# Optimization experiments

Hardware: AMD Instinct MI355X
Metric: run time of the kernel (lower is better)

Reference implementation:

```python
import jax, jax.numpy as jnp
import numpy as np

E = 64      # hidden_dim
FF = 128    # ff_dim
H = 4       # nhead
D = E // H  # head_dim = 16
STEPS = 16  # recursion_steps
IN = 200    # input_dim
B = 131072  # batch


def _ln(h, g, b):
    m = h.mean(-1, keepdims=True)
    v = ((h - m) ** 2).mean(-1, keepdims=True)
    return (h - m) * jax.lax.rsqrt(v + 1e-5) * g + b


def _ffn(h, w1, b1, w2, b2):
    return jax.nn.gelu(h @ w1.T + b1, approximate=False) @ w2.T + b2


def _forward(x, W_in, b_in, g_in, be_in,
             z_in_w, z_in_b, z_out_w, z_out_b,
             z_ffn_w1, z_ffn_b1, z_ffn_w2, z_ffn_b2,
             zn1_g, zn1_b, zn2_g, zn2_b,
             y_in_w, y_in_b, y_out_w, y_out_b,
             y_ffn_w1, y_ffn_b1, y_ffn_w2, y_ffn_b2,
             yn1_g, yn1_b, yn2_g, yn2_b,
             W_out, b_out):
    Bn = x.shape[0]
    x_proj = jax.nn.gelu(_ln(x @ W_in.T + b_in, g_in, be_in), approximate=False)  # [B,E]
    y0 = jnp.zeros((Bn, E), dtype=x.dtype)
    z0 = jnp.zeros((Bn, E), dtype=x.dtype)
    scale = 1.0 / np.sqrt(D).astype(np.float32)
    Wv_y = y_in_w[2 * E:]   # cross-attn over a single kv token: softmax weight == 1,
    bv_y = y_in_b[2 * E:]   # so output = out_proj(v_proj(z)) exactly (no approximation)

    def step(carry, _):
        y, z = carry
        seq = jnp.stack([x_proj, y, z], axis=1)            # [B,3,E]
        qkv = seq @ z_in_w.T + z_in_b                      # [B,3,3E]
        q, k, v = jnp.split(qkv, 3, axis=-1)
        rh = lambda t: t.reshape(Bn, 3, H, D).transpose(0, 2, 1, 3)  # [B,H,3,D]
        q, k, v = rh(q), rh(k), rh(v)
        att = jax.nn.softmax(jnp.einsum('bhsd,bhtd->bhst', q, k) * scale, axis=-1)
        o = jnp.einsum('bhst,bhtd->bhsd', att, v).transpose(0, 2, 1, 3).reshape(Bn, 3, E)
        o = o @ z_out_w.T + z_out_b
        z_res = _ln(z + o[:, 2, :], zn1_g, zn1_b)
        z2 = _ln(z_res + _ffn(z_res, z_ffn_w1, z_ffn_b1, z_ffn_w2, z_ffn_b2), zn2_g, zn2_b)
        ca = (z2 @ Wv_y.T + bv_y) @ y_out_w.T + y_out_b    # 1-token cross-attention
        y_res = _ln(y + ca, yn1_g, yn1_b)
        y2 = _ln(y_res + _ffn(y_res, y_ffn_w1, y_ffn_b1, y_ffn_w2, y_ffn_b2), yn2_g, yn2_b)
        return (y2, z2), None

    (y, z), _ = jax.lax.scan(step, (y0, z0), None, length=STEPS)
    return (y @ W_out.T + b_out)[:, 0]                     # [B]


def setup_inputs() -> dict:
    key = jax.random.key(0)
    ks = jax.random.split(key, 12)
    f = lambda k, s: jax.random.normal(k, s, dtype=jnp.float32) * 0.05
    zeros = lambda s: jnp.zeros(s, dtype=jnp.float32)
    ones = lambda s: jnp.ones(s, dtype=jnp.float32)
    return {
        'x': jax.random.normal(ks[0], (B, IN), dtype=jnp.float32),
        'W_in': f(ks[1], (E, IN)), 'b_in': zeros((E,)),
        'g_in': ones((E,)), 'be_in': zeros((E,)),
        'z_in_w': f(ks[2], (3 * E, E)), 'z_in_b': zeros((3 * E,)),
        'z_out_w': f(ks[3], (E, E)), 'z_out_b': zeros((E,)),
        'z_ffn_w1': f(ks[4], (FF, E)), 'z_ffn_b1': zeros((FF,)),
        'z_ffn_w2': f(ks[5], (E, FF)), 'z_ffn_b2': zeros((E,)),
        'zn1_g': ones((E,)), 'zn1_b': zeros((E,)),
        'zn2_g': ones((E,)), 'zn2_b': zeros((E,)),
        'y_in_w': f(ks[6], (3 * E, E)), 'y_in_b': zeros((3 * E,)),
        'y_out_w': f(ks[7], (E, E)), 'y_out_b': zeros((E,)),
        'y_ffn_w1': f(ks[8], (FF, E)), 'y_ffn_b1': zeros((FF,)),
        'y_ffn_w2': f(ks[9], (E, FF)), 'y_ffn_b2': zeros((E,)),
        'yn1_g': ones((E,)), 'yn1_b': zeros((E,)),
        'yn2_g': ones((E,)), 'yn2_b': zeros((E,)),
        'W_out': f(ks[10], (1, E)), 'b_out': zeros((1,)),
    }


def reference(x, W_in, b_in, g_in, be_in,
              z_in_w, z_in_b, z_out_w, z_out_b,
              z_ffn_w1, z_ffn_b1, z_ffn_w2, z_ffn_b2,
              zn1_g, zn1_b, zn2_g, zn2_b,
              y_in_w, y_in_b, y_out_w, y_out_b,
              y_ffn_w1, y_ffn_b1, y_ffn_w2, y_ffn_b2,
              yn1_g, yn1_b, yn2_g, yn2_b,
              W_out, b_out):
    return _forward(x, W_in, b_in, g_in, be_in,
                    z_in_w, z_in_b, z_out_w, z_out_b,
                    z_ffn_w1, z_ffn_b1, z_ffn_w2, z_ffn_b2,
                    zn1_g, zn1_b, zn2_g, zn2_b,
                    y_in_w, y_in_b, y_out_w, y_out_b,
                    y_ffn_w1, y_ffn_b1, y_ffn_w2, y_ffn_b2,
                    yn1_g, yn1_b, yn2_g, yn2_b,
                    W_out, b_out)
```

## Files before the change

### kernel.cpp

```cpp
#include <hip/hip_runtime.h>
#include <math.h>


constexpr int STEPS = 16;
constexpr int INDIM = 200;

typedef __attribute__((ext_vector_type(8))) short bfrag8;
typedef __attribute__((ext_vector_type(4))) float f32x4;
typedef __attribute__((ext_vector_type(4))) short s16x4;

constexpr int FB_WIN  = 0;
constexpr int NFRAG   = 140;
constexpr int NPARAM  = 1544;

constexpr int LB_ZQ   = 0;
constexpr int LB_ZK   = 8;
constexpr int LB_ZV   = 16;
constexpr int LB_ZOUT = 24;
constexpr int LB_ZF1  = 32;
constexpr int LB_ZF2  = 48;
constexpr int LB_YV   = 64;
constexpr int LB_YOUT = 72;
constexpr int LB_YF1  = 80;
constexpr int LB_YF2  = 96;
constexpr int NSTEADY = 112;

constexpr int PB_BIN   = 0;
constexpr int PB_GIN   = 64;
constexpr int PB_BEIN  = 128;
constexpr int PB_ZINB  = 192;
constexpr int PB_ZOUTB = 384;
constexpr int PB_ZF1B  = 448;
constexpr int PB_ZF2B  = 576;
constexpr int PB_ZN1G  = 640;
constexpr int PB_ZN1B  = 704;
constexpr int PB_ZN2G  = 768;
constexpr int PB_ZN2B  = 832;
constexpr int PB_YVB   = 896;
constexpr int PB_YOUTB = 960;
constexpr int PB_YF1B  = 1024;
constexpr int PB_YF2B  = 1152;
constexpr int PB_YN1G  = 1216;
constexpr int PB_YN1B  = 1280;
constexpr int PB_YN2G  = 1344;
constexpr int PB_YN2B  = 1408;
constexpr int PB_WOUT  = 1472;
constexpr int PB_BOUT  = 1536;

constexpr int S64      = 72;
constexpr int L_W      = 0;
constexpr int L_P      = 57344;
constexpr int L_ACT    = 60432;
constexpr int WAVE_SH  = 1152;
constexpr int NWAVE    = 16;
constexpr int ARENA_SH = L_ACT + NWAVE * WAVE_SH;

struct Params {
  const float *x, *W_in, *b_in, *g_in, *be_in;
  const float *z_in_w, *z_in_b, *z_out_w, *z_out_b;
  const float *z_ffn_w1, *z_ffn_b1, *z_ffn_w2, *z_ffn_b2;
  const float *zn1_g, *zn1_b, *zn2_g, *zn2_b;
  const float *y_in_w, *y_in_b, *y_out_w, *y_out_b;
  const float *y_ffn_w1, *y_ffn_b1, *y_ffn_w2, *y_ffn_b2;
  const float *yn1_g, *yn1_b, *yn2_g, *yn2_b;
  const float *W_out, *b_out;
  float *out;
  int nrows;
};

__device__ __forceinline__ ushort f2bf_rne(float f) {
  uint u = __float_as_uint(f);
  u += 0x7FFFu + ((u >> 16) & 1u);
  return (ushort)(u >> 16);
}

__device__ __forceinline__ ushort f2bf(float f) {
  return (ushort)((__float_as_uint(f) + 0x8000u) >> 16);
}
__device__ __forceinline__ uint pk2(float a, float b) {
  uint ua = __float_as_uint(a) + 0x8000u;
  uint ub = __float_as_uint(b) + 0x8000u;
  return (ua >> 16) | (ub & 0xFFFF0000u);
}
__device__ __forceinline__ float upk_lo(uint u) {
  return __uint_as_float(u << 16);
}
__device__ __forceinline__ float upk_hi(uint u) {
  return __uint_as_float(u & 0xFFFF0000u);
}
__device__ __forceinline__ f32x4 upk4(const uint* p) {
  f32x4 r;
  r.x = upk_lo(p[0]); r.y = upk_hi(p[0]);
  r.z = upk_lo(p[1]); r.w = upk_hi(p[1]);
  return r;
}
__device__ __forceinline__ float dot4(f32x4 a, f32x4 b) {
  return a.x * b.x + a.y * b.y + a.z * b.z + a.w * b.w;
}
__device__ __forceinline__ void stc(short* buf, int stride, int mt, int q,
                                    int s, f32x4 c) {
  s16x4 v;
  v.x = (short)f2bf(c.x); v.y = (short)f2bf(c.y);
  v.z = (short)f2bf(c.z); v.w = (short)f2bf(c.w);
  *(s16x4*)(buf + s * stride + mt * 16 + q * 4) = v;
}

__device__ __forceinline__ void c2b_p(const uint p[8], bfrag8& b0, bfrag8& b1,
                                      int lane) {
  const int srcA = (lane & 15) | ((lane & 16) << 1);
  const int srcB = srcA + 16;
  const bool odd = (lane & 32) != 0;
  uint ev0 = p[0], ev1 = p[1], ev2 = p[4], ev3 = p[5];
  uint od0 = p[2], od1 = p[3], od2 = p[6], od3 = p[7];
  uint rA0, rA1, rA2, rA3, rB0, rB1, rB2, rB3;
  {
    uint e, o;
    e = (uint)__shfl((int)ev0, srcA); o = (uint)__shfl((int)od0, srcA); rA0 = odd ? o : e;
    e = (uint)__shfl((int)ev1, srcA); o = (uint)__shfl((int)od1, srcA); rA1 = odd ? o : e;
    e = (uint)__shfl((int)ev2, srcA); o = (uint)__shfl((int)od2, srcA); rA2 = odd ? o : e;
    e = (uint)__shfl((int)ev3, srcA); o = (uint)__shfl((int)od3, srcA); rA3 = odd ? o : e;
    e = (uint)__shfl((int)ev0, srcB); o = (uint)__shfl((int)od0, srcB); rB0 = odd ? o : e;
    e = (uint)__shfl((int)ev1, srcB); o = (uint)__shfl((int)od1, srcB); rB1 = odd ? o : e;
    e = (uint)__shfl((int)ev2, srcB); o = (uint)__shfl((int)od2, srcB); rB2 = odd ? o : e;
    e = (uint)__shfl((int)ev3, srcB); o = (uint)__shfl((int)od3, srcB); rB3 = odd ? o : e;
  }
  union U { uint u[4]; bfrag8 b; };
  U u0, u1;
  u0.u[0] = rA0; u0.u[1] = rA1; u0.u[2] = rB0; u0.u[3] = rB1;
  u1.u[0] = rA2; u1.u[1] = rA3; u1.u[2] = rB2; u1.u[3] = rB3;
  b0 = u0.b; b1 = u1.b;
}
__device__ __forceinline__ void c2b(const f32x4 c[4], bfrag8& b0, bfrag8& b1,
                                    int lane) {
  uint p[8];
#pragma unroll
  for (int mt = 0; mt < 4; ++mt) {
    p[2 * mt]     = pk2(c[mt].x, c[mt].y);
    p[2 * mt + 1] = pk2(c[mt].z, c[mt].w);
  }
  c2b_p(p, b0, b1, lane);
}

template <int MT>
__device__ __forceinline__ void layerN2(const short* in0, const short* in1,
                                        const short* lw, int fbase,
                                        const float* bias, f32x4* c0, f32x4* c1,
                                        int lane, int q, int s) {
  bfrag8 b0[2], b1[2];
#pragma unroll
  for (int kt = 0; kt < 2; ++kt) {
    b0[kt] = *(const bfrag8*)(in0 + s * S64 + kt * 32 + q * 8);
    b1[kt] = *(const bfrag8*)(in1 + s * S64 + kt * 32 + q * 8);
  }
#pragma unroll
  for (int mt = 0; mt < MT; ++mt) {
    f32x4 b4 = *(const f32x4*)(bias + mt * 16 + q * 4);
    c0[mt] = b4; c1[mt] = b4;
  }
#pragma unroll
  for (int mt = 0; mt < MT; ++mt) {
#pragma unroll
    for (int kt = 0; kt < 2; ++kt) {
      bfrag8 af = *(const bfrag8*)(lw + (fbase + mt * 2 + kt) * 512 + lane * 8);
      c0[mt] = __builtin_amdgcn_mfma_f32_16x16x32_bf16(af, b0[kt], c0[mt], 0, 0, 0);
      c1[mt] = __builtin_amdgcn_mfma_f32_16x16x32_bf16(af, b1[kt], c1[mt], 0, 0, 0);
    }
  }
}

template <int MT>
__device__ __forceinline__ void layerB2(const bfrag8* bfA, const bfrag8* bfB,
                                        const short* lw, int fbase,
                                        const float* bias, f32x4* cA, f32x4* cB,
                                        int lane, int q) {
#pragma unroll
  for (int mt = 0; mt < MT; ++mt) {
    f32x4 b4 = *(const f32x4*)(bias + mt * 16 + q * 4);
    cA[mt] = b4; cB[mt] = b4;
  }
#pragma unroll
  for (int mt = 0; mt < MT; ++mt) {
#pragma unroll
    for (int kt = 0; kt < 2; ++kt) {
      bfrag8 af = *(const bfrag8*)(lw + (fbase + mt * 2 + kt) * 512 + lane * 8);
      cA[mt] = __builtin_amdgcn_mfma_f32_16x16x32_bf16(af, bfA[kt], cA[mt], 0, 0, 0);
      cB[mt] = __builtin_amdgcn_mfma_f32_16x16x32_bf16(af, bfB[kt], cB[mt], 0, 0, 0);
    }
  }
}

template <int MT>
__device__ __forceinline__ void layerB4(const bfrag8* bf0, const bfrag8* bf1,
                                        const bfrag8* bf2, const bfrag8* bf3,
                                        const short* lw, int fbase,
                                        const float* bias, f32x4* c0, f32x4* c1,
                                        f32x4* c2, f32x4* c3, int lane, int q) {
#pragma unroll
  for (int mt = 0; mt < MT; ++mt) {
    f32x4 b4 = *(const f32x4*)(bias + mt * 16 + q * 4);
    c0[mt] = b4; c1[mt] = b4; c2[mt] = b4; c3[mt] = b4;
  }
#pragma unroll
  for (int mt = 0; mt < MT; ++mt) {
#pragma unroll
    for (int kt = 0; kt < 2; ++kt) {
      bfrag8 af = *(const bfrag8*)(lw + (fbase + mt * 2 + kt) * 512 + lane * 8);
      c0[mt] = __builtin_amdgcn_mfma_f32_16x16x32_bf16(af, bf0[kt], c0[mt], 0, 0, 0);
      c1[mt] = __builtin_amdgcn_mfma_f32_16x16x32_bf16(af, bf1[kt], c1[mt], 0, 0, 0);
      c2[mt] = __builtin_amdgcn_mfma_f32_16x16x32_bf16(af, bf2[kt], c2[mt], 0, 0, 0);
      c3[mt] = __builtin_amdgcn_mfma_f32_16x16x32_bf16(af, bf3[kt], c3[mt], 0, 0, 0);
    }
  }
}

__device__ __forceinline__ void lnorm_c(f32x4 c[4], const float* g,
                                        const float* b, int q) {
  f32x4 s4 = (c[0] + c[1]) + (c[2] + c[3]);
  float sm = (s4.x + s4.y) + (s4.z + s4.w);
  sm += __shfl_xor(sm, 16); sm += __shfl_xor(sm, 32);
  float mean = sm * (1.f / 64.f);
  f32x4 vs4 = {0.f, 0.f, 0.f, 0.f};
#pragma unroll
  for (int mt = 0; mt < 4; ++mt) {
    f32x4 d = c[mt] - mean;
    c[mt] = d;
    vs4 = vs4 + d * d;
  }
  float vs = (vs4.x + vs4.y) + (vs4.z + vs4.w);
  vs += __shfl_xor(vs, 16); vs += __shfl_xor(vs, 32);
  float rs = rsqrtf(vs * (1.f / 64.f) + 1e-5f);
#pragma unroll
  for (int mt = 0; mt < 4; ++mt) {
    f32x4 g4 = *(const f32x4*)(g + mt * 16 + q * 4);
    f32x4 b4 = *(const f32x4*)(b + mt * 16 + q * 4);
    c[mt] = (c[mt] * rs) * g4 + b4;
  }
}

__device__ __forceinline__ f32x4 gelu4(f32x4 x) {
  const float K = 0.70710678118654752f;
  f32x4 ax;
  ax.x = fabsf(x.x) * K; ax.y = fabsf(x.y) * K;
  ax.z = fabsf(x.z) * K; ax.w = fabsf(x.w) * K;
  f32x4 u = ax * 0.47047f + 1.0f;
  f32x4 t;
  t.x = __builtin_amdgcn_rcpf(u.x); t.y = __builtin_amdgcn_rcpf(u.y);
  t.z = __builtin_amdgcn_rcpf(u.z); t.w = __builtin_amdgcn_rcpf(u.w);
  f32x4 poly = ((t * 0.7478556f + (-0.0958798f)) * t + 0.3480242f) * t;
  f32x4 gq = ax * ax;
  f32x4 e;
  e.x = __expf(-gq.x); e.y = __expf(-gq.y);
  e.z = __expf(-gq.z); e.w = __expf(-gq.w);
  f32x4 r = poly * e;
  f32x4 er;
  er.x = copysignf(1.0f - r.x, x.x); er.y = copysignf(1.0f - r.y, x.y);
  er.z = copysignf(1.0f - r.z, x.z); er.w = copysignf(1.0f - r.w, x.w);
  f32x4 h = x * 0.5f;
  return h + h * er;
}

__device__ __forceinline__ void ffn2_via_th2(const f32x4 h0[8], const f32x4 h1[8],
                                             short* TH0, short* TH1,
                                             const short* lw, int f2base,
                                             const float* b2, f32x4 c0[4],
                                             f32x4 c1[4], int lane, int q, int s) {
#pragma unroll
  for (int mt = 0; mt < 4; ++mt) {
    f32x4 b4 = *(const f32x4*)(b2 + mt * 16 + q * 4);
    c0[mt] = b4; c1[mt] = b4;
  }
#pragma unroll
  for (int g = 0; g < 2; ++g) {
#pragma unroll
    for (int mt = 0; mt < 4; ++mt) {
      stc(TH0, S64, mt, q, s, gelu4(h0[4 * g + mt]));
      stc(TH1, S64, mt, q, s, gelu4(h1[4 * g + mt]));
    }
    bfrag8 bf0[2], bf1[2];
#pragma unroll
    for (int kt = 0; kt < 2; ++kt) {
      bf0[kt] = *(const bfrag8*)(TH0 + s * S64 + kt * 32 + q * 8);
      bf1[kt] = *(const bfrag8*)(TH1 + s * S64 + kt * 32 + q * 8);
    }
#pragma unroll
    for (int mt = 0; mt < 4; ++mt) {
#pragma unroll
      for (int kt = 0; kt < 2; ++kt) {
        bfrag8 af =
            *(const bfrag8*)(lw + (f2base + mt * 4 + 2 * g + kt) * 512 + lane * 8);
        c0[mt] = __builtin_amdgcn_mfma_f32_16x16x32_bf16(af, bf0[kt], c0[mt], 0, 0, 0);
        c1[mt] = __builtin_amdgcn_mfma_f32_16x16x32_bf16(af, bf1[kt], c1[mt], 0, 0, 0);
      }
    }
  }
}

__global__ void prepack_kernel(Params p, ushort* wf) {
  int f = blockIdx.x;
  int lane = threadIdx.x;

  if (f == NFRAG) {
    float* pw = (float*)(wf + (size_t)NFRAG * 512);
    for (int t = lane; t < NPARAM; t += 64) {
      float v = 0.f;
      if      (t < 64)   v = p.b_in[t];
      else if (t < 128)  v = p.g_in[t - 64];
      else if (t < 192)  v = p.be_in[t - 128];
      else if (t < 384)  v = p.z_in_b[t - 192];
      else if (t < 448)  v = p.z_out_b[t - 384];
      else if (t < 576)  v = p.z_ffn_b1[t - 448];
      else if (t < 640)  v = p.z_ffn_b2[t - 576];
      else if (t < 704)  v = p.zn1_g[t - 640];
      else if (t < 768)  v = p.zn1_b[t - 704];
      else if (t < 832)  v = p.zn2_g[t - 768];
      else if (t < 896)  v = p.zn2_b[t - 832];
      else if (t < 960)  v = p.y_in_b[128 + t - 896];
      else if (t < 1024) v = p.y_out_b[t - 960];
      else if (t < 1152) v = p.y_ffn_b1[t - 1024];
      else if (t < 1216) v = p.y_ffn_b2[t - 1152];
      else if (t < 1280) v = p.yn1_g[t - 1216];
      else if (t < 1344) v = p.yn1_b[t - 1280];
      else if (t < 1408) v = p.yn2_g[t - 1344];
      else if (t < 1472) v = p.yn2_b[t - 1408];
      else if (t < 1536) v = p.W_out[t - 1472];
      else if (t == 1536) v = p.b_out[0];
      pw[t] = v;
    }
    return;
  }

  int q = lane >> 4, r = lane & 15;
  const float* src; int K, mt, kt, l;
  if (f < 28)        { src = p.W_in;                K = 200; mt = f / 7;  kt = f % 7; }
  else if (f < 36)   { l = f - 28;  src = p.z_in_w;            K = 64;  mt = l / 2; kt = l % 2; }
  else if (f < 44)   { l = f - 36;  src = p.z_in_w + 64 * 64;  K = 64;  mt = l / 2; kt = l % 2; }
  else if (f < 52)   { l = f - 44;  src = p.z_in_w + 128 * 64; K = 64;  mt = l / 2; kt = l % 2; }
  else if (f < 60)   { l = f - 52;  src = p.z_out_w;           K = 64;  mt = l / 2; kt = l % 2; }
  else if (f < 76)   { l = f - 60;  src = p.z_ffn_w1;          K = 64;  mt = l / 2; kt = l % 2; }
  else if (f < 92)   { l = f - 76;  src = p.z_ffn_w2;          K = 128; mt = l / 4; kt = l % 4; }
  else if (f < 100)  { l = f - 92;  src = p.y_in_w + 128 * 64; K = 64;  mt = l / 2; kt = l % 2; }
  else if (f < 108)  { l = f - 100; src = p.y_out_w;           K = 64;  mt = l / 2; kt = l % 2; }
  else if (f < 124)  { l = f - 108; src = p.y_ffn_w1;          K = 64;  mt = l / 2; kt = l % 2; }
  else               { l = f - 124; src = p.y_ffn_w2;          K = 128; mt = l / 4; kt = l % 4; }

  int row = mt * 16 + r;
  int col = kt * 32 + q * 8;
  bfrag8 o;
#pragma unroll
  for (int j = 0; j < 8; ++j) {
    int cc = col + j;
    float v = (cc < K) ? src[(size_t)row * K + cc] : 0.0f;
    o[j] = (short)f2bf_rne(v);
  }
  *(bfrag8*)(wf + (size_t)f * 512 + lane * 8) = o;
}

__global__ __launch_bounds__(512, 1)
void trm_mfma_kernel(Params p, const ushort* wf) {
  __shared__ __align__(16) short arena[ARENA_SH];
  const int tid = threadIdx.x;
  const int wave = tid >> 6, lane = tid & 63;
  const int q = lane >> 4, s = lane & 15;

  {
    const uint4* srcw = (const uint4*)(wf + (size_t)28 * 512);
    uint4* dstw = (uint4*)(arena + L_W);
    for (int i = tid; i < NSTEADY * 64; i += 512) dstw[i] = srcw[i];
    const uint4* srcp = (const uint4*)(wf + (size_t)NFRAG * 512);
    uint4* dstp = (uint4*)(arena + L_P);
    for (int i = tid; i < NPARAM / 4; i += 512) dstp[i] = srcp[i];
  }
  __syncthreads();

  const short* LW = arena + L_W;
  const float* P  = (const float*)(arena + L_P);
  short* TH0 = arena + L_ACT + (2 * wave) * WAVE_SH;
  short* TH1 = TH0 + WAVE_SH;

  const int chunks = (p.nrows + 255) / 256;
  for (int ic = blockIdx.x; ic < chunks; ic += gridDim.x) {
    int rw[2];
#pragma unroll
    for (int t = 0; t < 2; ++t) {
      int r = ic * 256 + wave * 16 + t * 128 + s;
      rw[t] = (r < p.nrows) ? r : (p.nrows - 1);
    }

    bfrag8 xpB[2][2];
    {
      bfrag8 xb[2][7];
#pragma unroll
      for (int t = 0; t < 2; ++t) {
        const float* xr = p.x + (size_t)rw[t] * INDIM;
#pragma unroll
        for (int kt = 0; kt < 7; ++kt) {
          int k0i = kt * 32 + q * 8;
          bfrag8 v;
          if (kt < 6 || q == 0) {
            f32x4 lo = *(const f32x4*)(xr + k0i);
            f32x4 hi = *(const f32x4*)(xr + k0i + 4);
            v[0] = (short)f2bf(lo.x); v[1] = (short)f2bf(lo.y);
            v[2] = (short)f2bf(lo.z); v[3] = (short)f2bf(lo.w);
            v[4] = (short)f2bf(hi.x); v[5] = (short)f2bf(hi.y);
            v[6] = (short)f2bf(hi.z); v[7] = (short)f2bf(hi.w);
          } else {
#pragma unroll
            for (int j = 0; j < 8; ++j) v[j] = 0;
          }
          xb[t][kt] = v;
        }
      }
      f32x4 c[2][4];
#pragma unroll
      for (int mt = 0; mt < 4; ++mt) {
        f32x4 b4 = *(const f32x4*)(P + PB_BIN + mt * 16 + q * 4);
        c[0][mt] = b4; c[1][mt] = b4;
      }
#pragma unroll
      for (int mt = 0; mt < 4; ++mt)
#pragma unroll
        for (int kt = 0; kt < 7; ++kt) {
          bfrag8 af =
              *(const bfrag8*)(wf + (size_t)(FB_WIN + mt * 7 + kt) * 512 + lane * 8);
          c[0][mt] = __builtin_amdgcn_mfma_f32_16x16x32_bf16(af, xb[0][kt], c[0][mt], 0, 0, 0);
          c[1][mt] = __builtin_amdgcn_mfma_f32_16x16x32_bf16(af, xb[1][kt], c[1][mt], 0, 0, 0);
        }
#pragma unroll
      for (int t = 0; t < 2; ++t) {
        lnorm_c(c[t], P + PB_GIN, P + PB_BEIN, q);
#pragma unroll
        for (int mt = 0; mt < 4; ++mt) c[t][mt] = gelu4(c[t][mt]);
        c2b(c[t], xpB[t][0], xpB[t][1], lane);
      }
    }

    uint k0p[2][8], v0p[2][8], zCp[2][8], yCp[2][8];
    bfrag8 zB[2][2], yB[2][2];
    {
      f32x4 ck[2][4], cv[2][4];
      layerB2<4>(xpB[0], xpB[1], LW, LB_ZK, P + PB_ZINB + 64, ck[0], ck[1], lane, q);
      layerB2<4>(xpB[0], xpB[1], LW, LB_ZV, P + PB_ZINB + 128, cv[0], cv[1], lane, q);
#pragma unroll
      for (int t = 0; t < 2; ++t) {
#pragma unroll
        for (int mt = 0; mt < 4; ++mt) {
          k0p[t][2 * mt]     = pk2(ck[t][mt].x, ck[t][mt].y);
          k0p[t][2 * mt + 1] = pk2(ck[t][mt].z, ck[t][mt].w);
          v0p[t][2 * mt]     = pk2(cv[t][mt].x, cv[t][mt].y);
          v0p[t][2 * mt + 1] = pk2(cv[t][mt].z, cv[t][mt].w);
          zCp[t][2 * mt] = 0u; zCp[t][2 * mt + 1] = 0u;
          yCp[t][2 * mt] = 0u; yCp[t][2 * mt + 1] = 0u;
        }
#pragma unroll
        for (int kt = 0; kt < 2; ++kt) {
          bfrag8 zr0;
#pragma unroll
          for (int j = 0; j < 8; ++j) zr0[j] = 0;
          zB[t][kt] = zr0; yB[t][kt] = zr0;
        }
      }
    }

    for (int st = 0; st < STEPS; ++st) {
      float w0[2][4], w1[2][4], w2[2][4], wi[2][4];
      {
        f32x4 q2[2][4], kz[2][4], ky[2][4];
        layerB2<4>(zB[0], zB[1], LW, LB_ZQ, P + PB_ZINB, q2[0], q2[1], lane, q);
        layerB4<4>(zB[0], yB[0], zB[1], yB[1], LW, LB_ZK, P + PB_ZINB + 64,
                   kz[0], ky[0], kz[1], ky[1], lane, q);
#pragma unroll
        for (int t = 0; t < 2; ++t) {
#pragma unroll
          for (int mt = 0; mt < 4; ++mt) {
            float a0 = dot4(q2[t][mt], upk4(k0p[t] + 2 * mt));
            float a1 = dot4(q2[t][mt], ky[t][mt]);
            float a2 = dot4(q2[t][mt], kz[t][mt]);
            a0 += __shfl_xor(a0, 16); a0 += __shfl_xor(a0, 32);
            a1 += __shfl_xor(a1, 16); a1 += __shfl_xor(a1, 32);
            a2 += __shfl_xor(a2, 16); a2 += __shfl_xor(a2, 32);
            a0 *= 0.25f; a1 *= 0.25f; a2 *= 0.25f;
            float mx = fmaxf(a0, fmaxf(a1, a2));
            float e0 = __expf(a0 - mx), e1 = __expf(a1 - mx), e2 = __expf(a2 - mx);
            w0[t][mt] = e0; w1[t][mt] = e1; w2[t][mt] = e2;
            wi[t][mt] = __builtin_amdgcn_rcpf(e0 + e1 + e2);
          }
        }
      }
      {
        f32x4 vz[2][4], vy[2][4];
        layerB4<4>(zB[0], yB[0], zB[1], yB[1], LW, LB_ZV, P + PB_ZINB + 128,
                   vz[0], vy[0], vz[1], vy[1], lane, q);
#pragma unroll
        for (int mt = 0; mt < 4; ++mt) {
          f32x4 o0 = (upk4(v0p[0] + 2 * mt) * w0[0][mt] + vy[0][mt] * w1[0][mt] +
                      vz[0][mt] * w2[0][mt]) * wi[0][mt];
          stc(TH0, S64, mt, q, s, o0);
          f32x4 o1 = (upk4(v0p[1] + 2 * mt) * w0[1][mt] + vy[1][mt] * w1[1][mt] +
                      vz[1][mt] * w2[1][mt]) * wi[1][mt];
          stc(TH1, S64, mt, q, s, o1);
        }
      }

      uint zrp[2][8];
      {
        f32x4 zr[2][4];
        layerN2<4>(TH0, TH1, LW, LB_ZOUT, P + PB_ZOUTB, zr[0], zr[1], lane, q, s);
#pragma unroll
        for (int t = 0; t < 2; ++t) {
#pragma unroll
          for (int mt = 0; mt < 4; ++mt) zr[t][mt] = zr[t][mt] + upk4(zCp[t] + 2 * mt);
          lnorm_c(zr[t], P + PB_ZN1G, P + PB_ZN1B, q);
        }
#pragma unroll
        for (int mt = 0; mt < 4; ++mt) {
          stc(TH0, S64, mt, q, s, zr[0][mt]);
          stc(TH1, S64, mt, q, s, zr[1][mt]);
        }
#pragma unroll
        for (int t = 0; t < 2; ++t)
#pragma unroll
          for (int mt = 0; mt < 4; ++mt) {
            zrp[t][2 * mt]     = pk2(zr[t][mt].x, zr[t][mt].y);
            zrp[t][2 * mt + 1] = pk2(zr[t][mt].z, zr[t][mt].w);
          }
      }

      f32x4 z2[2][4];
      {
        f32x4 h8[2][8];
        layerN2<8>(TH0, TH1, LW, LB_ZF1, P + PB_ZF1B, h8[0], h8[1], lane, q, s);
        ffn2_via_th2(h8[0], h8[1], TH0, TH1, LW, LB_ZF2, P + PB_ZF2B,
                     z2[0], z2[1], lane, q, s);
      }
#pragma unroll
      for (int t = 0; t < 2; ++t) {
#pragma unroll
        for (int mt = 0; mt < 4; ++mt) z2[t][mt] = z2[t][mt] + upk4(zrp[t] + 2 * mt);
        lnorm_c(z2[t], P + PB_ZN2G, P + PB_ZN2B, q);
        uint zp[8];
#pragma unroll
        for (int mt = 0; mt < 4; ++mt) {
          zp[2 * mt]     = pk2(z2[t][mt].x, z2[t][mt].y);
          zp[2 * mt + 1] = pk2(z2[t][mt].z, z2[t][mt].w);
          zCp[t][2 * mt] = zp[2 * mt]; zCp[t][2 * mt + 1] = zp[2 * mt + 1];
        }
        c2b_p(zp, zB[t][0], zB[t][1], lane);
      }

      {
        f32x4 t4[2][4];
        layerB2<4>(zB[0], zB[1], LW, LB_YV, P + PB_YVB, t4[0], t4[1], lane, q);
#pragma unroll
        for (int mt = 0; mt < 4; ++mt) {
          stc(TH0, S64, mt, q, s, t4[0][mt]);
          stc(TH1, S64, mt, q, s, t4[1][mt]);
        }
      }

      uint yrp[2][8];
      {
        f32x4 yr[2][4];
        layerN2<4>(TH0, TH1, LW, LB_YOUT, P + PB_YOUTB, yr[0], yr[1], lane, q, s);
#pragma unroll
        for (int t = 0; t < 2; ++t) {
#pragma unroll
          for (int mt = 0; mt < 4; ++mt) yr[t][mt] = yr[t][mt] + upk4(yCp[t] + 2 * mt);
          lnorm_c(yr[t], P + PB_YN1G, P + PB_YN1B, q);
        }
#pragma unroll
        for (int mt = 0; mt < 4; ++mt) {
          stc(TH0, S64, mt, q, s, yr[0][mt]);
          stc(TH1, S64, mt, q, s, yr[1][mt]);
        }
#pragma unroll
        for (int t = 0; t < 2; ++t)
#pragma unroll
          for (int mt = 0; mt < 4; ++mt) {
            yrp[t][2 * mt]     = pk2(yr[t][mt].x, yr[t][mt].y);
            yrp[t][2 * mt + 1] = pk2(yr[t][mt].z, yr[t][mt].w);
          }
      }

      f32x4 y2[2][4];
      {
        f32x4 h8[2][8];
        layerN2<8>(TH0, TH1, LW, LB_YF1, P + PB_YF1B, h8[0], h8[1], lane, q, s);
        ffn2_via_th2(h8[0], h8[1], TH0, TH1, LW, LB_YF2, P + PB_YF2B,
                     y2[0], y2[1], lane, q, s);
      }
#pragma unroll
      for (int t = 0; t < 2; ++t) {
#pragma unroll
        for (int mt = 0; mt < 4; ++mt) y2[t][mt] = y2[t][mt] + upk4(yrp[t] + 2 * mt);
        lnorm_c(y2[t], P + PB_YN2G, P + PB_YN2B, q);
        uint yp[8];
#pragma unroll
        for (int mt = 0; mt < 4; ++mt) {
          yp[2 * mt]     = pk2(y2[t][mt].x, y2[t][mt].y);
          yp[2 * mt + 1] = pk2(y2[t][mt].z, y2[t][mt].w);
          yCp[t][2 * mt] = yp[2 * mt]; yCp[t][2 * mt + 1] = yp[2 * mt + 1];
        }
        c2b_p(yp, yB[t][0], yB[t][1], lane);
      }
    }

#pragma unroll
    for (int t = 0; t < 2; ++t) {
      float acc = 0.f;
#pragma unroll
      for (int mt = 0; mt < 4; ++mt) {
        f32x4 w4 = *(const f32x4*)(P + PB_WOUT + mt * 16 + q * 4);
        acc += dot4(upk4(yCp[t] + 2 * mt), w4);
      }
      acc += __shfl_xor(acc, 16); acc += __shfl_xor(acc, 32);
      int orow = ic * 256 + wave * 16 + t * 128 + s;
      if (q == 0 && orow < p.nrows) p.out[orow] = acc + P[PB_BOUT];
    }
  }
}

extern "C" void kernel_launch(void* const* d_in, const int* in_sizes, int n_in,
                              void* d_out, int out_size, void* d_ws,
                              size_t ws_size, hipStream_t stream) {
  Params p;
  const float* const* in = (const float* const*)d_in;
  p.x        = in[0];  p.W_in     = in[1];  p.b_in     = in[2];
  p.g_in     = in[3];  p.be_in    = in[4];
  p.z_in_w   = in[5];  p.z_in_b   = in[6];
  p.z_out_w  = in[7];  p.z_out_b  = in[8];
  p.z_ffn_w1 = in[9];  p.z_ffn_b1 = in[10];
  p.z_ffn_w2 = in[11]; p.z_ffn_b2 = in[12];
  p.zn1_g    = in[13]; p.zn1_b    = in[14];
  p.zn2_g    = in[15]; p.zn2_b    = in[16];
  p.y_in_w   = in[17]; p.y_in_b   = in[18];
  p.y_out_w  = in[19]; p.y_out_b  = in[20];
  p.y_ffn_w1 = in[21]; p.y_ffn_b1 = in[22];
  p.y_ffn_w2 = in[23]; p.y_ffn_b2 = in[24];
  p.yn1_g    = in[25]; p.yn1_b    = in[26];
  p.yn2_g    = in[27]; p.yn2_b    = in[28];
  p.W_out    = in[29]; p.b_out    = in[30];
  p.out      = (float*)d_out;
  p.nrows    = in_sizes[0] / INDIM;

  if (ws_size < (size_t)NFRAG * 1024 + NPARAM * 4) return;
  ushort* wf = (ushort*)d_ws;

  hipLaunchKernelGGL(prepack_kernel, dim3(NFRAG + 1), dim3(64), 0, stream, p, wf);
  hipLaunchKernelGGL(trm_mfma_kernel, dim3(256), dim3(512), 0, stream, p, wf);
}
```

Before: 876.3 us.

## Double threads per block, halve per-wave LDS staging, fuse FFN layers per group

Blocks grow to 1024 threads with each wave owning one LDS staging tile instead of two. Each block now covers 512 rows per chunk. Of the two row tiles each wave processes, one still goes through LDS and the other is converted in registers with cross-lane shuffles. The FFN is restructured to compute the first layer in groups of 64 hidden units and feed each group straight into the second layer, which cuts peak register use. The goal is more waves for latency hiding at the cost of extra shuffle work, and it risks register spills under the tighter launch bound.

```diff
diff --git a/kernel.cpp b/kernel.cpp
--- a/kernel.cpp
+++ b/kernel.cpp
@@ -97,6 +97,13 @@
 __device__ __forceinline__ float dot4(f32x4 a, f32x4 b) {
   return a.x * b.x + a.y * b.y + a.z * b.z + a.w * b.w;
 }
+__device__ __forceinline__ void pk8(const f32x4 c[4], uint p[8]) {
+#pragma unroll
+  for (int mt = 0; mt < 4; ++mt) {
+    p[2 * mt]     = pk2(c[mt].x, c[mt].y);
+    p[2 * mt + 1] = pk2(c[mt].z, c[mt].w);
+  }
+}
 __device__ __forceinline__ void stc(short* buf, int stride, int mt, int q,
                                     int s, f32x4 c) {
   s16x4 v;
@@ -130,28 +137,16 @@
   u1.u[0] = rA2; u1.u[1] = rA3; u1.u[2] = rB2; u1.u[3] = rB3;
   b0 = u0.b; b1 = u1.b;
 }
-__device__ __forceinline__ void c2b(const f32x4 c[4], bfrag8& b0, bfrag8& b1,
-                                    int lane) {
-  uint p[8];
-#pragma unroll
-  for (int mt = 0; mt < 4; ++mt) {
-    p[2 * mt]     = pk2(c[mt].x, c[mt].y);
-    p[2 * mt + 1] = pk2(c[mt].z, c[mt].w);
-  }
-  c2b_p(p, b0, b1, lane);
-}
 
 template <int MT>
-__device__ __forceinline__ void layerN2(const short* in0, const short* in1,
+__device__ __forceinline__ void layerNR(const short* th, const bfrag8* b1,
                                         const short* lw, int fbase,
                                         const float* bias, f32x4* c0, f32x4* c1,
                                         int lane, int q, int s) {
-  bfrag8 b0[2], b1[2];
-#pragma unroll
-  for (int kt = 0; kt < 2; ++kt) {
-    b0[kt] = *(const bfrag8*)(in0 + s * S64 + kt * 32 + q * 8);
-    b1[kt] = *(const bfrag8*)(in1 + s * S64 + kt * 32 + q * 8);
-  }
+  bfrag8 b0[2];
+#pragma unroll
+  for (int kt = 0; kt < 2; ++kt)
+    b0[kt] = *(const bfrag8*)(th + s * S64 + kt * 32 + q * 8);
 #pragma unroll
   for (int mt = 0; mt < MT; ++mt) {
     f32x4 b4 = *(const f32x4*)(bias + mt * 16 + q * 4);
@@ -185,30 +180,6 @@
       bfrag8 af = *(const bfrag8*)(lw + (fbase + mt * 2 + kt) * 512 + lane * 8);
       cA[mt] = __builtin_amdgcn_mfma_f32_16x16x32_bf16(af, bfA[kt], cA[mt], 0, 0, 0);
       cB[mt] = __builtin_amdgcn_mfma_f32_16x16x32_bf16(af, bfB[kt], cB[mt], 0, 0, 0);
-    }
-  }
-}
-
-template <int MT>
-__device__ __forceinline__ void layerB4(const bfrag8* bf0, const bfrag8* bf1,
-                                        const bfrag8* bf2, const bfrag8* bf3,
-                                        const short* lw, int fbase,
-                                        const float* bias, f32x4* c0, f32x4* c1,
-                                        f32x4* c2, f32x4* c3, int lane, int q) {
-#pragma unroll
-  for (int mt = 0; mt < MT; ++mt) {
-    f32x4 b4 = *(const f32x4*)(bias + mt * 16 + q * 4);
-    c0[mt] = b4; c1[mt] = b4; c2[mt] = b4; c3[mt] = b4;
-  }
-#pragma unroll
-  for (int mt = 0; mt < MT; ++mt) {
-#pragma unroll
-    for (int kt = 0; kt < 2; ++kt) {
-      bfrag8 af = *(const bfrag8*)(lw + (fbase + mt * 2 + kt) * 512 + lane * 8);
-      c0[mt] = __builtin_amdgcn_mfma_f32_16x16x32_bf16(af, bf0[kt], c0[mt], 0, 0, 0);
-      c1[mt] = __builtin_amdgcn_mfma_f32_16x16x32_bf16(af, bf1[kt], c1[mt], 0, 0, 0);
-      c2[mt] = __builtin_amdgcn_mfma_f32_16x16x32_bf16(af, bf2[kt], c2[mt], 0, 0, 0);
-      c3[mt] = __builtin_amdgcn_mfma_f32_16x16x32_bf16(af, bf3[kt], c3[mt], 0, 0, 0);
     }
   }
 }
@@ -259,11 +230,15 @@
   return h + h * er;
 }
 
-__device__ __forceinline__ void ffn2_via_th2(const f32x4 h0[8], const f32x4 h1[8],
-                                             short* TH0, short* TH1,
-                                             const short* lw, int f2base,
-                                             const float* b2, f32x4 c0[4],
-                                             f32x4 c1[4], int lane, int q, int s) {
+__device__ __forceinline__ void ffn_dual(short* TH, const bfrag8 rB1[2],
+                                         const short* lw, int f1base, int f2base,
+                                         const float* b1, const float* b2,
+                                         f32x4 c0[4], f32x4 c1[4],
+                                         int lane, int q, int s) {
+  bfrag8 b0[2];
+#pragma unroll
+  for (int kt = 0; kt < 2; ++kt)
+    b0[kt] = *(const bfrag8*)(TH + s * S64 + kt * 32 + q * 8);
 #pragma unroll
   for (int mt = 0; mt < 4; ++mt) {
     f32x4 b4 = *(const f32x4*)(b2 + mt * 16 + q * 4);
@@ -271,25 +246,44 @@
   }
 #pragma unroll
   for (int g = 0; g < 2; ++g) {
-#pragma unroll
-    for (int mt = 0; mt < 4; ++mt) {
-      stc(TH0, S64, mt, q, s, gelu4(h0[4 * g + mt]));
-      stc(TH1, S64, mt, q, s, gelu4(h1[4 * g + mt]));
-    }
-    bfrag8 bf0[2], bf1[2];
-#pragma unroll
-    for (int kt = 0; kt < 2; ++kt) {
-      bf0[kt] = *(const bfrag8*)(TH0 + s * S64 + kt * 32 + q * 8);
-      bf1[kt] = *(const bfrag8*)(TH1 + s * S64 + kt * 32 + q * 8);
-    }
-#pragma unroll
-    for (int mt = 0; mt < 4; ++mt) {
+    f32x4 h0[4], h1[4];
+#pragma unroll
+    for (int m = 0; m < 4; ++m) {
+      f32x4 b4 = *(const f32x4*)(b1 + (4 * g + m) * 16 + q * 4);
+      h0[m] = b4; h1[m] = b4;
+    }
+#pragma unroll
+    for (int m = 0; m < 4; ++m) {
 #pragma unroll
       for (int kt = 0; kt < 2; ++kt) {
         bfrag8 af =
-            *(const bfrag8*)(lw + (f2base + mt * 4 + 2 * g + kt) * 512 + lane * 8);
-        c0[mt] = __builtin_amdgcn_mfma_f32_16x16x32_bf16(af, bf0[kt], c0[mt], 0, 0, 0);
-        c1[mt] = __builtin_amdgcn_mfma_f32_16x16x32_bf16(af, bf1[kt], c1[mt], 0, 0, 0);
+            *(const bfrag8*)(lw + (f1base + (4 * g + m) * 2 + kt) * 512 + lane * 8);
+        h0[m] = __builtin_amdgcn_mfma_f32_16x16x32_bf16(af, b0[kt], h0[m], 0, 0, 0);
+        h1[m] = __builtin_amdgcn_mfma_f32_16x16x32_bf16(af, rB1[kt], h1[m], 0, 0, 0);
+      }
+    }
+    uint ph[8];
+#pragma unroll
+    for (int m = 0; m < 4; ++m) {
+      h0[m] = gelu4(h0[m]);
+      h1[m] = gelu4(h1[m]);
+      stc(TH, S64, m, q, s, h0[m]);
+      ph[2 * m]     = pk2(h1[m].x, h1[m].y);
+      ph[2 * m + 1] = pk2(h1[m].z, h1[m].w);
+    }
+    bfrag8 t0[2], hB1[2];
+#pragma unroll
+    for (int kt = 0; kt < 2; ++kt)
+      t0[kt] = *(const bfrag8*)(TH + s * S64 + kt * 32 + q * 8);
+    c2b_p(ph, hB1[0], hB1[1], lane);
+#pragma unroll
+    for (int m = 0; m < 4; ++m) {
+#pragma unroll
+      for (int kt = 0; kt < 2; ++kt) {
+        bfrag8 af =
+            *(const bfrag8*)(lw + (f2base + m * 4 + 2 * g + kt) * 512 + lane * 8);
+        c0[m] = __builtin_amdgcn_mfma_f32_16x16x32_bf16(af, t0[kt], c0[m], 0, 0, 0);
+        c1[m] = __builtin_amdgcn_mfma_f32_16x16x32_bf16(af, hB1[kt], c1[m], 0, 0, 0);
       }
     }
   }
@@ -355,7 +349,7 @@
   *(bfrag8*)(wf + (size_t)f * 512 + lane * 8) = o;
 }
 
-__global__ __launch_bounds__(512, 1)
+__global__ __launch_bounds__(1024, 1)
 void trm_mfma_kernel(Params p, const ushort* wf) {
   __shared__ __align__(16) short arena[ARENA_SH];
   const int tid = threadIdx.x;
@@ -365,28 +359,27 @@
   {
     const uint4* srcw = (const uint4*)(wf + (size_t)28 * 512);
     uint4* dstw = (uint4*)(arena + L_W);
-    for (int i = tid; i < NSTEADY * 64; i += 512) dstw[i] = srcw[i];
+    for (int i = tid; i < NSTEADY * 64; i += 1024) dstw[i] = srcw[i];
     const uint4* srcp = (const uint4*)(wf + (size_t)NFRAG * 512);
     uint4* dstp = (uint4*)(arena + L_P);
-    for (int i = tid; i < NPARAM / 4; i += 512) dstp[i] = srcp[i];
+    for (int i = tid; i < NPARAM / 4; i += 1024) dstp[i] = srcp[i];
   }
   __syncthreads();
 
   const short* LW = arena + L_W;
   const float* P  = (const float*)(arena + L_P);
-  short* TH0 = arena + L_ACT + (2 * wave) * WAVE_SH;
-  short* TH1 = TH0 + WAVE_SH;
-
-  const int chunks = (p.nrows + 255) / 256;
+  short* TH = arena + L_ACT + wave * WAVE_SH;
+
+  const int chunks = (p.nrows + 511) / 512;
   for (int ic = blockIdx.x; ic < chunks; ic += gridDim.x) {
     int rw[2];
 #pragma unroll
     for (int t = 0; t < 2; ++t) {
-      int r = ic * 256 + wave * 16 + t * 128 + s;
+      int r = ic * 512 + wave * 16 + t * 256 + s;
       rw[t] = (r < p.nrows) ? r : (p.nrows - 1);
     }
 
-    bfrag8 xpB[2][2];
+    bfrag8 xpB0[2], xpB1[2];
     {
       bfrag8 xb[2][7];
 #pragma unroll
@@ -410,11 +403,11 @@
           xb[t][kt] = v;
         }
       }
-      f32x4 c[2][4];
+      f32x4 c0[4], c1[4];
 #pragma unroll
       for (int mt = 0; mt < 4; ++mt) {
         f32x4 b4 = *(const f32x4*)(P + PB_BIN + mt * 16 + q * 4);
-        c[0][mt] = b4; c[1][mt] = b4;
+        c0[mt] = b4; c1[mt] = b4;
       }
 #pragma unroll
       for (int mt = 0; mt < 4; ++mt)
@@ -422,26 +415,27 @@
         for (int kt = 0; kt < 7; ++kt) {
           bfrag8 af =
               *(const bfrag8*)(wf + (size_t)(FB_WIN + mt * 7 + kt) * 512 + lane * 8);
-          c[0][mt] = __builtin_amdgcn_mfma_f32_16x16x32_bf16(af, xb[0][kt], c[0][mt], 0, 0, 0);
-          c[1][mt] = __builtin_amdgcn_mfma_f32_16x16x32_bf16(af, xb[1][kt], c[1][mt], 0, 0, 0);
+          c0[mt] = __builtin_amdgcn_mfma_f32_16x16x32_bf16(af, xb[0][kt], c0[mt], 0, 0, 0);
+          c1[mt] = __builtin_amdgcn_mfma_f32_16x16x32_bf16(af, xb[1][kt], c1[mt], 0, 0, 0);
         }
-#pragma unroll
-      for (int t = 0; t < 2; ++t) {
-        lnorm_c(c[t], P + PB_GIN, P + PB_BEIN, q);
-#pragma unroll
-        for (int mt = 0; mt < 4; ++mt) c[t][mt] = gelu4(c[t][mt]);
-        c2b(c[t], xpB[t][0], xpB[t][1], lane);
-      }
+      lnorm_c(c0, P + PB_GIN, P + PB_BEIN, q);
+      lnorm_c(c1, P + PB_GIN, P + PB_BEIN, q);
+#pragma unroll
+      for (int mt = 0; mt < 4; ++mt) { c0[mt] = gelu4(c0[mt]); c1[mt] = gelu4(c1[mt]); }
+      uint p0[8], p1[8];
+      pk8(c0, p0); pk8(c1, p1);
+      c2b_p(p0, xpB0[0], xpB0[1], lane);
+      c2b_p(p1, xpB1[0], xpB1[1], lane);
     }
 
     uint k0p[2][8], v0p[2][8], zCp[2][8], yCp[2][8];
-    bfrag8 zB[2][2], yB[2][2];
+    bfrag8 zB0[2], zB1[2], yB0[2], yB1[2];
     {
       f32x4 ck[2][4], cv[2][4];
-      layerB2<4>(xpB[0], xpB[1], LW, LB_ZK, P + PB_ZINB + 64, ck[0], ck[1], lane, q);
-      layerB2<4>(xpB[0], xpB[1], LW, LB_ZV, P + PB_ZINB + 128, cv[0], cv[1], lane, q);
-#pragma unroll
-      for (int t = 0; t < 2; ++t) {
+      layerB2<4>(xpB0, xpB1, LW, LB_ZK, P + PB_ZINB + 64, ck[0], ck[1], lane, q);
+      layerB2<4>(xpB0, xpB1, LW, LB_ZV, P + PB_ZINB + 128, cv[0], cv[1], lane, q);
+#pragma unroll
+      for (int t = 0; t < 2; ++t)
 #pragma unroll
         for (int mt = 0; mt < 4; ++mt) {
           k0p[t][2 * mt]     = pk2(ck[t][mt].x, ck[t][mt].y);
@@ -451,13 +445,12 @@
           zCp[t][2 * mt] = 0u; zCp[t][2 * mt + 1] = 0u;
           yCp[t][2 * mt] = 0u; yCp[t][2 * mt + 1] = 0u;
         }
-#pragma unroll
-        for (int kt = 0; kt < 2; ++kt) {
-          bfrag8 zr0;
-#pragma unroll
-          for (int j = 0; j < 8; ++j) zr0[j] = 0;
-          zB[t][kt] = zr0; yB[t][kt] = zr0;
-        }
+      bfrag8 z0;
+#pragma unroll
+      for (int j = 0; j < 8; ++j) z0[j] = 0;
+#pragma unroll
+      for (int kt = 0; kt < 2; ++kt) {
+        zB0[kt] = z0; zB1[kt] = z0; yB0[kt] = z0; yB1[kt] = z0;
       }
     }
 
@@ -465,11 +458,11 @@
       float w0[2][4], w1[2][4], w2[2][4], wi[2][4];
       {
         f32x4 q2[2][4], kz[2][4], ky[2][4];
-        layerB2<4>(zB[0], zB[1], LW, LB_ZQ, P + PB_ZINB, q2[0], q2[1], lane, q);
-        layerB4<4>(zB[0], yB[0], zB[1], yB[1], LW, LB_ZK, P + PB_ZINB + 64,
-                   kz[0], ky[0], kz[1], ky[1], lane, q);
-#pragma unroll
-        for (int t = 0; t < 2; ++t) {
+        layerB2<4>(zB0, zB1, LW, LB_ZQ, P + PB_ZINB, q2[0], q2[1], lane, q);
+        layerB2<4>(zB0, zB1, LW, LB_ZK, P + PB_ZINB + 64, kz[0], kz[1], lane, q);
+        layerB2<4>(yB0, yB1, LW, LB_ZK, P + PB_ZINB + 64, ky[0], ky[1], lane, q);
+#pragma unroll
+        for (int t = 0; t < 2; ++t)
 #pragma unroll
           for (int mt = 0; mt < 4; ++mt) {
             float a0 = dot4(q2[t][mt], upk4(k0p[t] + 2 * mt));
@@ -484,123 +477,111 @@
             w0[t][mt] = e0; w1[t][mt] = e1; w2[t][mt] = e2;
             wi[t][mt] = __builtin_amdgcn_rcpf(e0 + e1 + e2);
           }
-        }
-      }
+      }
+      bfrag8 oB1[2];
       {
         f32x4 vz[2][4], vy[2][4];
-        layerB4<4>(zB[0], yB[0], zB[1], yB[1], LW, LB_ZV, P + PB_ZINB + 128,
-                   vz[0], vy[0], vz[1], vy[1], lane, q);
+        layerB2<4>(zB0, zB1, LW, LB_ZV, P + PB_ZINB + 128, vz[0], vz[1], lane, q);
+        layerB2<4>(yB0, yB1, LW, LB_ZV, P + PB_ZINB + 128, vy[0], vy[1], lane, q);
+        uint op1[8];
 #pragma unroll
         for (int mt = 0; mt < 4; ++mt) {
           f32x4 o0 = (upk4(v0p[0] + 2 * mt) * w0[0][mt] + vy[0][mt] * w1[0][mt] +
                       vz[0][mt] * w2[0][mt]) * wi[0][mt];
-          stc(TH0, S64, mt, q, s, o0);
+          stc(TH, S64, mt, q, s, o0);
           f32x4 o1 = (upk4(v0p[1] + 2 * mt) * w0[1][mt] + vy[1][mt] * w1[1][mt] +
                       vz[1][mt] * w2[1][mt]) * wi[1][mt];
-          stc(TH1, S64, mt, q, s, o1);
+          op1[2 * mt]     = pk2(o1.x, o1.y);
+          op1[2 * mt + 1] = pk2(o1.z, o1.w);
         }
+        c2b_p(op1, oB1[0], oB1[1], lane);
       }
 
       uint zrp[2][8];
+      bfrag8 zrB1[2];
       {
-        f32x4 zr[2][4];
-        layerN2<4>(TH0, TH1, LW, LB_ZOUT, P + PB_ZOUTB, zr[0], zr[1], lane, q, s);
-#pragma unroll
-        for (int t = 0; t < 2; ++t) {
-#pragma unroll
-          for (int mt = 0; mt < 4; ++mt) zr[t][mt] = zr[t][mt] + upk4(zCp[t] + 2 * mt);
-          lnorm_c(zr[t], P + PB_ZN1G, P + PB_ZN1B, q);
+        f32x4 zr0[4], zr1[4];
+        layerNR<4>(TH, oB1, LW, LB_ZOUT, P + PB_ZOUTB, zr0, zr1, lane, q, s);
+#pragma unroll
+        for (int mt = 0; mt < 4; ++mt) {
+          zr0[mt] = zr0[mt] + upk4(zCp[0] + 2 * mt);
+          zr1[mt] = zr1[mt] + upk4(zCp[1] + 2 * mt);
         }
+        lnorm_c(zr0, P + PB_ZN1G, P + PB_ZN1B, q);
+        lnorm_c(zr1, P + PB_ZN1G, P + PB_ZN1B, q);
+#pragma unroll
+        for (int mt = 0; mt < 4; ++mt) stc(TH, S64, mt, q, s, zr0[mt]);
+        pk8(zr0, zrp[0]);
+        pk8(zr1, zrp[1]);
+        c2b_p(zrp[1], zrB1[0], zrB1[1], lane);
+      }
+
+      f32x4 z20[4], z21[4];
+      ffn_dual(TH, zrB1, LW, LB_ZF1, LB_ZF2, P + PB_ZF1B, P + PB_ZF2B,
+               z20, z21, lane, q, s);
+#pragma unroll
+      for (int mt = 0; mt < 4; ++mt) {
+        z20[mt] = z20[mt] + upk4(zrp[0] + 2 * mt);
+        z21[mt] = z21[mt] + upk4(zrp[1] + 2 * mt);
+      }
+      lnorm_c(z20, P + PB_ZN2G, P + PB_ZN2B, q);
+      lnorm_c(z21, P + PB_ZN2G, P + PB_ZN2B, q);
+      {
+        uint zp0[8], zp1[8];
+        pk8(z20, zp0); pk8(z21, zp1);
+#pragma unroll
+        for (int i = 0; i < 8; ++i) { zCp[0][i] = zp0[i]; zCp[1][i] = zp1[i]; }
+        c2b_p(zp0, zB0[0], zB0[1], lane);
+        c2b_p(zp1, zB1[0], zB1[1], lane);
+      }
+
+      bfrag8 tB1[2];
+      {
+        f32x4 t40[4], t41[4];
+        layerB2<4>(zB0, zB1, LW, LB_YV, P + PB_YVB, t40, t41, lane, q);
+        uint t41p[8];
+#pragma unroll
+        for (int mt = 0; mt < 4; ++mt) stc(TH, S64, mt, q, s, t40[mt]);
+        pk8(t41, t41p);
+        c2b_p(t41p, tB1[0], tB1[1], lane);
+      }
+
+      uint yrp[2][8];
+      bfrag8 yrB1[2];
+      {
+        f32x4 yr0[4], yr1[4];
+        layerNR<4>(TH, tB1, LW, LB_YOUT, P + PB_YOUTB, yr0, yr1, lane, q, s);
 #pragma unroll
         for (int mt = 0; mt < 4; ++mt) {
-          stc(TH0, S64, mt, q, s, zr[0][mt]);
-          stc(TH1, S64, mt, q, s, zr[1][mt]);
+          yr0[mt] = yr0[mt] + upk4(yCp[0] + 2 * mt);
+          yr1[mt] = yr1[mt] + upk4(yCp[1] + 2 * mt);
         }
-#pragma unroll
-        for (int t = 0; t < 2; ++t)
-#pragma unroll
-          for (int mt = 0; mt < 4; ++mt) {
-            zrp[t][2 * mt]     = pk2(zr[t][mt].x, zr[t][mt].y);
-            zrp[t][2 * mt + 1] = pk2(zr[t][mt].z, zr[t][mt].w);
-          }
-      }
-
-      f32x4 z2[2][4];
+        lnorm_c(yr0, P + PB_YN1G, P + PB_YN1B, q);
+        lnorm_c(yr1, P + PB_YN1G, P + PB_YN1B, q);
+#pragma unroll
+        for (int mt = 0; mt < 4; ++mt) stc(TH, S64, mt, q, s, yr0[mt]);
+        pk8(yr0, yrp[0]);
+        pk8(yr1, yrp[1]);
+        c2b_p(yrp[1], yrB1[0], yrB1[1], lane);
+      }
+
+      f32x4 y20[4], y21[4];
+      ffn_dual(TH, yrB1, LW, LB_YF1, LB_YF2, P + PB_YF1B, P + PB_YF2B,
+               y20, y21, lane, q, s);
+#pragma unroll
+      for (int mt = 0; mt < 4; ++mt) {
+        y20[mt] = y20[mt] + upk4(yrp[0] + 2 * mt);
+        y21[mt] = y21[mt] + upk4(yrp[1] + 2 * mt);
+      }
+      lnorm_c(y20, P + PB_YN2G, P + PB_YN2B, q);
+      lnorm_c(y21, P + PB_YN2G, P + PB_YN2B, q);
       {
-        f32x4 h8[2][8];
-        layerN2<8>(TH0, TH1, LW, LB_ZF1, P + PB_ZF1B, h8[0], h8[1], lane, q, s);
-        ffn2_via_th2(h8[0], h8[1], TH0, TH1, LW, LB_ZF2, P + PB_ZF2B,
-                     z2[0], z2[1], lane, q, s);
-      }
-#pragma unroll
-      for (int t = 0; t < 2; ++t) {
-#pragma unroll
-        for (int mt = 0; mt < 4; ++mt) z2[t][mt] = z2[t][mt] + upk4(zrp[t] + 2 * mt);
-        lnorm_c(z2[t], P + PB_ZN2G, P + PB_ZN2B, q);
-        uint zp[8];
-#pragma unroll
-        for (int mt = 0; mt < 4; ++mt) {
-          zp[2 * mt]     = pk2(z2[t][mt].x, z2[t][mt].y);
-          zp[2 * mt + 1] = pk2(z2[t][mt].z, z2[t][mt].w);
-          zCp[t][2 * mt] = zp[2 * mt]; zCp[t][2 * mt + 1] = zp[2 * mt + 1];
-        }
-        c2b_p(zp, zB[t][0], zB[t][1], lane);
-      }
-
-      {
-        f32x4 t4[2][4];
-        layerB2<4>(zB[0], zB[1], LW, LB_YV, P + PB_YVB, t4[0], t4[1], lane, q);
-#pragma unroll
-        for (int mt = 0; mt < 4; ++mt) {
-          stc(TH0, S64, mt, q, s, t4[0][mt]);
-          stc(TH1, S64, mt, q, s, t4[1][mt]);
-        }
-      }
-
-      uint yrp[2][8];
-      {
-        f32x4 yr[2][4];
-        layerN2<4>(TH0, TH1, LW, LB_YOUT, P + PB_YOUTB, yr[0], yr[1], lane, q, s);
-#pragma unroll
-        for (int t = 0; t < 2; ++t) {
-#pragma unroll
-          for (int mt = 0; mt < 4; ++mt) yr[t][mt] = yr[t][mt] + upk4(yCp[t] + 2 * mt);
-          lnorm_c(yr[t], P + PB_YN1G, P + PB_YN1B, q);
-        }
-#pragma unroll
-        for (int mt = 0; mt < 4; ++mt) {
-          stc(TH0, S64, mt, q, s, yr[0][mt]);
-          stc(TH1, S64, mt, q, s, yr[1][mt]);
-        }
-#pragma unroll
-        for (int t = 0; t < 2; ++t)
-#pragma unroll
-          for (int mt = 0; mt < 4; ++mt) {
-            yrp[t][2 * mt]     = pk2(yr[t][mt].x, yr[t][mt].y);
-            yrp[t][2 * mt + 1] = pk2(yr[t][mt].z, yr[t][mt].w);
-          }
-      }
-
-      f32x4 y2[2][4];
-      {
-        f32x4 h8[2][8];
-        layerN2<8>(TH0, TH1, LW, LB_YF1, P + PB_YF1B, h8[0], h8[1], lane, q, s);
-        ffn2_via_th2(h8[0], h8[1], TH0, TH1, LW, LB_YF2, P + PB_YF2B,
-                     y2[0], y2[1], lane, q, s);
-      }
-#pragma unroll
-      for (int t = 0; t < 2; ++t) {
-#pragma unroll
-        for (int mt = 0; mt < 4; ++mt) y2[t][mt] = y2[t][mt] + upk4(yrp[t] + 2 * mt);
-        lnorm_c(y2[t], P + PB_YN2G, P + PB_YN2B, q);
-        uint yp[8];
-#pragma unroll
-        for (int mt = 0; mt < 4; ++mt) {
-          yp[2 * mt]     = pk2(y2[t][mt].x, y2[t][mt].y);
-          yp[2 * mt + 1] = pk2(y2[t][mt].z, y2[t][mt].w);
-          yCp[t][2 * mt] = yp[2 * mt]; yCp[t][2 * mt + 1] = yp[2 * mt + 1];
-        }
-        c2b_p(yp, yB[t][0], yB[t][1], lane);
+        uint yp0[8], yp1[8];
+        pk8(y20, yp0); pk8(y21, yp1);
+#pragma unroll
+        for (int i = 0; i < 8; ++i) { yCp[0][i] = yp0[i]; yCp[1][i] = yp1[i]; }
+        c2b_p(yp0, yB0[0], yB0[1], lane);
+        c2b_p(yp1, yB1[0], yB1[1], lane);
       }
     }
 
@@ -613,7 +594,7 @@
         acc += dot4(upk4(yCp[t] + 2 * mt), w4);
       }
       acc += __shfl_xor(acc, 16); acc += __shfl_xor(acc, 32);
-      int orow = ic * 256 + wave * 16 + t * 128 + s;
+      int orow = ic * 512 + wave * 16 + t * 256 + s;
       if (q == 0 && orow < p.nrows) p.out[orow] = acc + P[PB_BOUT];
     }
   }
@@ -646,5 +627,5 @@
   ushort* wf = (ushort*)d_ws;
 
   hipLaunchKernelGGL(prepack_kernel, dim3(NFRAG + 1), dim3(64), 0, stream, p, wf);
-  hipLaunchKernelGGL(trm_mfma_kernel, dim3(256), dim3(512), 0, stream, p, wf);
-}
+  hipLaunchKernelGGL(trm_mfma_kernel, dim3(256), dim3(1024), 0, stream, p, wf);
+}
```

Measured after the change: 1.219 ms. 39.1% more time.
